# Kernel optimization log

Measured on AMD Instinct MI355X. Metric: run time of the kernel, lower is better.

Reference implementation:

```python
import jax, jax.numpy as jnp
import numpy as np

N = 50000      # num nodes
E = 800000     # num edges
F = 64         # in_channels
H = 4          # heads
C = 64         # out_channels
NEG_SLOPE = 0.2
SCALE = float(np.sqrt(F))  # scaled_product=True -> divide by sqrt(in_channels)


def setup_inputs() -> dict:
    key = jax.random.key(0)
    k1, k2, k3, k4, k5, k6 = jax.random.split(key, 6)
    x = jax.random.normal(k1, (N, F), dtype=jnp.float32)
    edge_index = jax.random.randint(k2, (2, E), 0, N, dtype=jnp.int32)
    edge_weight = jax.random.uniform(k3, (E, 1), dtype=jnp.float32)
    # learned parameters (glorot-ish scale)
    W_lin = jax.random.normal(k4, (F, H * C), dtype=jnp.float32) / np.sqrt(F)
    W_att = jax.random.normal(k5, (F, H * F), dtype=jnp.float32) / np.sqrt(F)
    bias = jnp.zeros((H * C,), dtype=jnp.float32)
    return {"x": x, "edge_index": edge_index, "edge_weight": edge_weight,
            "W_lin": W_lin, "W_att": W_att, "bias": bias}


def reference(x, edge_index, edge_weight, W_lin, W_att, bias):
    src = edge_index[0]  # j: source / message sender
    dst = edge_index[1]  # i: target / aggregation index

    # node transforms
    xs = (x @ W_lin).reshape(N, H, C)   # lin(x): values for messages
    u = (x @ W_att).reshape(N, H, F)    # lin_att(x): multiplicative attention keys

    # multiplicative attention score: x_j^T W_h x_i  -> [E, H]
    score = jnp.einsum('ehf,ef->eh', u[src], x[dst]) / SCALE
    score = jax.nn.leaky_relu(score, NEG_SLOPE)

    # masked scatter-softmax over incoming edges of each destination node
    smax = jax.ops.segment_max(jax.lax.stop_gradient(score), dst, num_segments=N)  # [N, H]
    e = jnp.exp(score - smax[dst]) * edge_weight                                   # mask = edge_weight
    denom = jax.ops.segment_sum(e, dst, num_segments=N) + 1e-16                    # [N, H]
    alpha = e / denom[dst]                                                         # [E, H]

    # message = alpha * x_src, aggregate (add) at destination
    out = jax.ops.segment_sum(alpha[:, :, None] * xs[src], dst, num_segments=N)    # [N, H, C]
    out = out.reshape(N, H * C) + bias                                             # concat heads + bias
    return out
```

## Files before the change

kernel.cpp:

```cpp
#include <hip/hip_runtime.h>
#include <hip/hip_bf16.h>
#include <math.h>

#define N_NODES 50000
#define N_EDGES 800000
#define GEMM_ROWS 32
#define AGG_NODES 32
#define CSR_STRIDE 64
#define SCAT_BLOCKS ((N_EDGES + 1023) / 1024)
#define QGEMM_BLOCKS ((N_NODES + GEMM_ROWS - 1) / GEMM_ROWS)
#define SCALE_FOLD 0.18033688011112042f
#define XT_STRIDE 34

typedef __attribute__((ext_vector_type(8))) short bf16x8_t;
typedef __attribute__((ext_vector_type(4))) float f32x4_t;

static __device__ __forceinline__ ushort bfrn(float v) {
  __hip_bfloat16 b = __float2bfloat16(v);
  return __builtin_bit_cast(ushort, b);
}
static __device__ __forceinline__ bf16x8_t as_bf16x8(uint4 u) {
  union { uint4 a; bf16x8_t b; } c; c.a = u; return c.b;
}
static __device__ __forceinline__ float bflo(uint u) {
  return __uint_as_float(u << 16);
}
static __device__ __forceinline__ float bfhi(uint u) {
  return __uint_as_float(u & 0xFFFF0000u);
}

__global__ __launch_bounds__(256) void init_kernel(
    int* __restrict__ deg, const float* __restrict__ Watt,
    float* __restrict__ Wt) {
  int i = blockIdx.x * 256 + threadIdx.x;
  if (i < N_NODES) deg[i] = 0;
  if (i < 16384) {
    int c = i & 63;
    int r = (i >> 6) & 63;
    int h = i >> 12;
    Wt[i] = Watt[c * 256 + h * 64 + r] * SCALE_FOLD;
  }
}

__global__ __launch_bounds__(256) void combo_kernel(
    const int* __restrict__ srcv, const int* __restrict__ dstv,
    const float* __restrict__ ew, int* __restrict__ deg,
    int2* __restrict__ csr2, const float* __restrict__ x,
    const float* __restrict__ Wt, uint2* __restrict__ q_t2,
    ushort* __restrict__ xhi) {
  const int tid = threadIdx.x;
  if (blockIdx.x < SCAT_BLOCKS) {
    const int e0 = blockIdx.x * 1024 + tid * 4;
    if (e0 + 3 < N_EDGES) {
      const int4 d4 = *(const int4*)(dstv + e0);
      const int4 s4 = *(const int4*)(srcv + e0);
      const float4 w4 = *(const float4*)(ew + e0);
      int p0 = atomicAdd(&deg[d4.x], 1);
      int p1 = atomicAdd(&deg[d4.y], 1);
      int p2 = atomicAdd(&deg[d4.z], 1);
      int p3 = atomicAdd(&deg[d4.w], 1);
      p0 = min(p0, CSR_STRIDE - 1);
      p1 = min(p1, CSR_STRIDE - 1);
      p2 = min(p2, CSR_STRIDE - 1);
      p3 = min(p3, CSR_STRIDE - 1);
      csr2[(size_t)d4.x * CSR_STRIDE + p0] =
          make_int2(s4.x, __float_as_int(w4.x));
      csr2[(size_t)d4.y * CSR_STRIDE + p1] =
          make_int2(s4.y, __float_as_int(w4.y));
      csr2[(size_t)d4.z * CSR_STRIDE + p2] =
          make_int2(s4.z, __float_as_int(w4.z));
      csr2[(size_t)d4.w * CSR_STRIDE + p3] =
          make_int2(s4.w, __float_as_int(w4.w));
    }
    return;
  }
  __shared__ float xlds[GEMM_ROWS * 64];
  const int blk = blockIdx.x - SCAT_BLOCKS;
#pragma unroll
  for (int p = 0; p < 8; ++p) {
    int idx = p * 256 + tid;
    int gidx = blk * (GEMM_ROWS * 64) + idx;
    xlds[idx] = (gidx < N_NODES * 64) ? x[gidx] : 0.f;
  }
  __syncthreads();
  {
    int row = tid >> 3;
    int c0 = (tid & 7) * 8;
    int grow = blk * GEMM_ROWS + row;
    if (grow < N_NODES) {
      uint hu[4];
#pragma unroll
      for (int d2 = 0; d2 < 4; ++d2) {
        float v0 = xlds[row * 64 + c0 + 2 * d2];
        float v1 = xlds[row * 64 + c0 + 2 * d2 + 1];
        hu[d2] = (uint)bfrn(v0) | ((uint)bfrn(v1) << 16);
      }
      *(uint4*)(xhi + (size_t)grow * 64 + c0) =
          make_uint4(hu[0], hu[1], hu[2], hu[3]);
    }
  }
  const int c4 = tid & 63;
  const int h = c4 >> 4;
  const int f4 = c4 & 15;
  const int rg = (tid >> 6) * 8;
  const float4* Wv = (const float4*)Wt;
  float4 acc[8] = {};
  for (int g = 0; g < 64; ++g) {
    float4 w4 = Wv[(size_t)h * 1024 + g * 16 + f4];
#pragma unroll
    for (int r = 0; r < 8; ++r) {
      float a = xlds[(rg + r) * 64 + g];
      acc[r].x += a * w4.x; acc[r].y += a * w4.y;
      acc[r].z += a * w4.z; acc[r].w += a * w4.w;
    }
  }
#pragma unroll
  for (int r = 0; r < 8; ++r) {
    int row = blk * GEMM_ROWS + rg + r;
    if (row < N_NODES) {
      uint2 pk;
      pk.x = (uint)bfrn(acc[r].x) | ((uint)bfrn(acc[r].y) << 16);
      pk.y = (uint)bfrn(acc[r].z) | ((uint)bfrn(acc[r].w) << 16);
      q_t2[(size_t)row * 64 + c4] = pk;
    }
  }
}

__global__ __launch_bounds__(256) void aggregate_kernel(
    const uint4* __restrict__ qt4, const uint4* __restrict__ xhi4,
    const int* __restrict__ deg, const int2* __restrict__ csr2,
    ushort* __restrict__ agg) {
  __shared__ __attribute__((aligned(16))) ushort xt16[4][16][XT_STRIDE * 2];
  __shared__ __attribute__((aligned(16))) ushort pt[4][4][16];
  const int wave = threadIdx.x >> 6;
  const int node = blockIdx.x * 4 + wave;
  const int lane = threadIdx.x & 63;
  const int l15 = lane & 15;
  const int lg = lane >> 4;
  const int hq = l15 & 3;

  const bf16x8_t Qa = as_bf16x8(qt4[(size_t)node * 32 + hq * 8 + lg]);
  const bf16x8_t Qb = as_bf16x8(qt4[(size_t)node * 32 + hq * 8 + 4 + lg]);
  int d = deg[node];
  d = min(d, CSR_STRIDE);
  const int ntiles = (d + 15) >> 4;
  const int s0 = node * CSR_STRIDE;

  const bf16x8_t ONES =
      as_bf16x8(make_uint4(0x3F803F80u, 0x3F803F80u, 0x3F803F80u, 0x3F803F80u));
  f32x4_t acc0 = {0.f, 0.f, 0.f, 0.f};
  f32x4_t acc1 = {0.f, 0.f, 0.f, 0.f};
  f32x4_t acc2 = {0.f, 0.f, 0.f, 0.f};
  f32x4_t acc3 = {0.f, 0.f, 0.f, 0.f};
  f32x4_t accL = {0.f, 0.f, 0.f, 0.f};
  const int eb = (lg & 1) * 8;

  for (int t = 0; t < ntiles; ++t) {
    const int k0 = s0 + t * 16;
    const int2 e2 = csr2[k0 + l15];
    const bool valid = (t * 16 + l15) < d;
    const float w = valid ? __int_as_float(e2.y) : 0.f;
    const uint j = min((uint)e2.x, (uint)(N_NODES - 1));
    const uint4 ah0 = xhi4[(size_t)j * 8 + lg];
    const uint4 ah1 = xhi4[(size_t)j * 8 + 4 + lg];
    {
      ushort* xr = &xt16[wave][l15][0];
      *(uint2*)(xr + 8 * lg) = make_uint2(ah0.x, ah0.y);
      *(uint2*)(xr + 8 * lg + 4) = make_uint2(ah0.z, ah0.w);
      *(uint2*)(xr + 32 + 8 * lg) = make_uint2(ah1.x, ah1.y);
      *(uint2*)(xr + 32 + 8 * lg + 4) = make_uint2(ah1.z, ah1.w);
    }
    f32x4_t S = {0.f, 0.f, 0.f, 0.f};
    S = __builtin_amdgcn_mfma_f32_16x16x32_bf16(Qa, as_bf16x8(ah0), S, 0, 0, 0);
    S = __builtin_amdgcn_mfma_f32_16x16x32_bf16(Qb, as_bf16x8(ah1), S, 0, 0, 0);
    float p0 = exp2f(fmaxf(S[0], 0.2f * S[0])) * w;
    float p1 = exp2f(fmaxf(S[1], 0.2f * S[1])) * w;
    float p2 = exp2f(fmaxf(S[2], 0.2f * S[2])) * w;
    float p3 = exp2f(fmaxf(S[3], 0.2f * S[3])) * w;
    if (lg == 0) {
      pt[wave][0][l15] = bfrn(p0);
      pt[wave][1][l15] = bfrn(p1);
      pt[wave][2][l15] = bfrn(p2);
      pt[wave][3][l15] = bfrn(p3);
    }
    uint4 pau = make_uint4(0u, 0u, 0u, 0u);
    if (lg < 2) pau = *(const uint4*)&pt[wave][hq][8 * lg];
    const bf16x8_t pa = as_bf16x8(pau);
#pragma unroll
    for (int b = 0; b < 4; ++b) {
      const int fc = 16 * b + l15;
      uint bw0 = (uint)xt16[wave][eb + 0][fc] |
                 ((uint)xt16[wave][eb + 1][fc] << 16);
      uint bw1 = (uint)xt16[wave][eb + 2][fc] |
                 ((uint)xt16[wave][eb + 3][fc] << 16);
      uint bw2 = (uint)xt16[wave][eb + 4][fc] |
                 ((uint)xt16[wave][eb + 5][fc] << 16);
      uint bw3 = (uint)xt16[wave][eb + 6][fc] |
                 ((uint)xt16[wave][eb + 7][fc] << 16);
      const bf16x8_t bx = as_bf16x8(make_uint4(bw0, bw1, bw2, bw3));
      if (b == 0)
        acc0 = __builtin_amdgcn_mfma_f32_16x16x32_bf16(pa, bx, acc0, 0, 0, 0);
      else if (b == 1)
        acc1 = __builtin_amdgcn_mfma_f32_16x16x32_bf16(pa, bx, acc1, 0, 0, 0);
      else if (b == 2)
        acc2 = __builtin_amdgcn_mfma_f32_16x16x32_bf16(pa, bx, acc2, 0, 0, 0);
      else
        acc3 = __builtin_amdgcn_mfma_f32_16x16x32_bf16(pa, bx, acc3, 0, 0, 0);
    }
    accL = __builtin_amdgcn_mfma_f32_16x16x32_bf16(pa, ONES, accL, 0, 0, 0);
  }

  const float lpv = (lg == 0) ? accL[0]
                  : (lg == 1) ? accL[1]
                  : (lg == 2) ? accL[2] : accL[3];
  const float inv = 1.f / (lpv + 1e-16f);
  const float v0 = ((lg == 0) ? acc0[0] : (lg == 1) ? acc0[1]
                   : (lg == 2) ? acc0[2] : acc0[3]) * inv;
  const float v1 = ((lg == 0) ? acc1[0] : (lg == 1) ? acc1[1]
                   : (lg == 2) ? acc1[2] : acc1[3]) * inv;
  const float v2 = ((lg == 0) ? acc2[0] : (lg == 1) ? acc2[1]
                   : (lg == 2) ? acc2[2] : acc2[3]) * inv;
  const float v3 = ((lg == 0) ? acc3[0] : (lg == 1) ? acc3[1]
                   : (lg == 2) ? acc3[2] : acc3[3]) * inv;
  ushort* ap = agg + (size_t)node * 256 + lg * 64 + l15;
  ap[0] = bfrn(v0);
  ap[16] = bfrn(v1);
  ap[32] = bfrn(v2);
  ap[48] = bfrn(v3);
}

__global__ __launch_bounds__(256) void out_gemm_kernel(
    const ushort* __restrict__ agg, const float* __restrict__ Wlin,
    const float* __restrict__ bias, float* __restrict__ out) {
  __shared__ float4 atile[AGG_NODES][4][17];
  const int tid = threadIdx.x;
  const int node0 = blockIdx.x * AGG_NODES;
  const uint2* av = (const uint2*)agg;
#pragma unroll
  for (int p = 0; p < 8; ++p) {
    int idx = p * 256 + tid;
    int row = idx >> 6;
    int cc = idx & 63;
    if (node0 + row < N_NODES) {
      uint2 u = av[(size_t)(node0 + row) * 64 + cc];
      float4 f;
      f.x = bflo(u.x); f.y = bfhi(u.x);
      f.z = bflo(u.y); f.w = bfhi(u.y);
      atile[row][cc >> 4][cc & 15] = f;
    }
  }
  __syncthreads();
  const int c4 = tid & 63;
  const int ns = tid >> 6;
  const int hh = c4 >> 4;
  const float4* Wv = (const float4*)Wlin;
  float4 acc[8] = {};
  for (int g4 = 0; g4 < 16; ++g4) {
    float4 w0 = Wv[(size_t)(g4 * 4 + 0) * 64 + c4];
    float4 w1 = Wv[(size_t)(g4 * 4 + 1) * 64 + c4];
    float4 w2 = Wv[(size_t)(g4 * 4 + 2) * 64 + c4];
    float4 w3 = Wv[(size_t)(g4 * 4 + 3) * 64 + c4];
#pragma unroll
    for (int n = 0; n < 8; ++n) {
      float4 a = atile[ns * 8 + n][hh][g4];
      acc[n].x += a.x * w0.x + a.y * w1.x + a.z * w2.x + a.w * w3.x;
      acc[n].y += a.x * w0.y + a.y * w1.y + a.z * w2.y + a.w * w3.y;
      acc[n].z += a.x * w0.z + a.y * w1.z + a.z * w2.z + a.w * w3.z;
      acc[n].w += a.x * w0.w + a.y * w1.w + a.z * w2.w + a.w * w3.w;
    }
  }
  float4 bv = ((const float4*)bias)[c4];
#pragma unroll
  for (int n = 0; n < 8; ++n) {
    int node = node0 + ns * 8 + n;
    if (node < N_NODES) {
      float4 o;
      o.x = acc[n].x + bv.x; o.y = acc[n].y + bv.y;
      o.z = acc[n].z + bv.z; o.w = acc[n].w + bv.w;
      ((float4*)out)[(size_t)node * 64 + c4] = o;
    }
  }
}

extern "C" void kernel_launch(void* const* d_in, const int* in_sizes, int n_in,
                              void* d_out, int out_size, void* d_ws,
                              size_t ws_size, hipStream_t stream) {
  (void)in_sizes; (void)n_in; (void)out_size; (void)ws_size;
  const float* x    = (const float*)d_in[0];
  const int*   ei   = (const int*)d_in[1];
  const float* ew   = (const float*)d_in[2];
  const float* Wlin = (const float*)d_in[3];
  const float* Watt = (const float*)d_in[4];
  const float* bias = (const float*)d_in[5];
  float* out = (float*)d_out;

  const int* srcv = ei;
  const int* dstv = ei + N_EDGES;

  char* ws = (char*)d_ws;
  size_t off = 0;
  auto alloc = [&](size_t bytes) {
    void* p = ws + off;
    off += (bytes + 255) & ~(size_t)255;
    return p;
  };
  ushort* q_t  = (ushort*)alloc((size_t)N_NODES * 256 * 2);
  ushort* agg  = (ushort*)alloc((size_t)N_NODES * 256 * 2);
  ushort* xhi  = (ushort*)alloc((size_t)N_NODES * 64 * 2);
  int2*   csr2 = (int2*)alloc((size_t)N_NODES * CSR_STRIDE * 8);
  int*    deg  = (int*)alloc((size_t)N_NODES * 4);
  float*  Wt   = (float*)alloc((size_t)64 * 256 * 4);

  init_kernel<<<(N_NODES + 255) / 256, 256, 0, stream>>>(deg, Watt, Wt);
  combo_kernel<<<SCAT_BLOCKS + QGEMM_BLOCKS, 256, 0, stream>>>(
      srcv, dstv, ew, deg, csr2, x, Wt, (uint2*)q_t, xhi);
  aggregate_kernel<<<N_NODES / 4, 256, 0, stream>>>(
      (const uint4*)q_t, (const uint4*)xhi, deg, csr2, agg);
  out_gemm_kernel<<<(N_NODES + AGG_NODES - 1) / AGG_NODES, 256, 0, stream>>>(
      agg, Wlin, bias, out);
}
```

Before: 159.5 us.

## Pack CSR source index and fp16 weight into one word; split scatter and qgemm

Each CSR entry shrinks from an 8-byte (int src, float weight) pair to a 4-byte word: a 16-bit source index plus an fp16 edge weight. This halves the bytes written by the scatter and read by the aggregation. The fused scatter/q-GEMM kernel is split into two separate launches, which gives up their overlap inside one grid. The q-GEMM inner loop now reads four x values per float4 LDS access. The 16-bit index only works because N_NODES is below 65536, and fp16 weights lose some precision.

```diff
diff --git a/kernel.cpp b/kernel.cpp
--- a/kernel.cpp
+++ b/kernel.cpp
@@ -27,6 +27,13 @@
 }
 static __device__ __forceinline__ float bfhi(uint u) {
   return __uint_as_float(u & 0xFFFF0000u);
+}
+static __device__ __forceinline__ uint pack_sw(int s, float w) {
+  ushort hw = __builtin_bit_cast(ushort, (_Float16)w);
+  return (uint)s | ((uint)hw << 16);
+}
+static __device__ __forceinline__ float unpack_w(uint pk) {
+  return (float)__builtin_bit_cast(_Float16, (ushort)(pk >> 16));
 }
 
 __global__ __launch_bounds__(256) void init_kernel(
@@ -42,40 +49,35 @@
   }
 }
 
-__global__ __launch_bounds__(256) void combo_kernel(
+__global__ __launch_bounds__(256) void scatter_kernel(
     const int* __restrict__ srcv, const int* __restrict__ dstv,
     const float* __restrict__ ew, int* __restrict__ deg,
-    int2* __restrict__ csr2, const float* __restrict__ x,
-    const float* __restrict__ Wt, uint2* __restrict__ q_t2,
-    ushort* __restrict__ xhi) {
+    uint* __restrict__ csr_p) {
+  const int e0 = blockIdx.x * 1024 + threadIdx.x * 4;
+  if (e0 + 3 >= N_EDGES) return;
+  const int4 d4 = *(const int4*)(dstv + e0);
+  const int4 s4 = *(const int4*)(srcv + e0);
+  const float4 w4 = *(const float4*)(ew + e0);
+  int p0 = atomicAdd(&deg[d4.x], 1);
+  int p1 = atomicAdd(&deg[d4.y], 1);
+  int p2 = atomicAdd(&deg[d4.z], 1);
+  int p3 = atomicAdd(&deg[d4.w], 1);
+  p0 = min(p0, CSR_STRIDE - 1);
+  p1 = min(p1, CSR_STRIDE - 1);
+  p2 = min(p2, CSR_STRIDE - 1);
+  p3 = min(p3, CSR_STRIDE - 1);
+  csr_p[(size_t)d4.x * CSR_STRIDE + p0] = pack_sw(s4.x, w4.x);
+  csr_p[(size_t)d4.y * CSR_STRIDE + p1] = pack_sw(s4.y, w4.y);
+  csr_p[(size_t)d4.z * CSR_STRIDE + p2] = pack_sw(s4.z, w4.z);
+  csr_p[(size_t)d4.w * CSR_STRIDE + p3] = pack_sw(s4.w, w4.w);
+}
+
+__global__ __launch_bounds__(256) void qgemm_kernel(
+    const float* __restrict__ x, const float* __restrict__ Wt,
+    uint2* __restrict__ q_t2, ushort* __restrict__ xhi) {
+  __shared__ float xlds[GEMM_ROWS * 64];
   const int tid = threadIdx.x;
-  if (blockIdx.x < SCAT_BLOCKS) {
-    const int e0 = blockIdx.x * 1024 + tid * 4;
-    if (e0 + 3 < N_EDGES) {
-      const int4 d4 = *(const int4*)(dstv + e0);
-      const int4 s4 = *(const int4*)(srcv + e0);
-      const float4 w4 = *(const float4*)(ew + e0);
-      int p0 = atomicAdd(&deg[d4.x], 1);
-      int p1 = atomicAdd(&deg[d4.y], 1);
-      int p2 = atomicAdd(&deg[d4.z], 1);
-      int p3 = atomicAdd(&deg[d4.w], 1);
-      p0 = min(p0, CSR_STRIDE - 1);
-      p1 = min(p1, CSR_STRIDE - 1);
-      p2 = min(p2, CSR_STRIDE - 1);
-      p3 = min(p3, CSR_STRIDE - 1);
-      csr2[(size_t)d4.x * CSR_STRIDE + p0] =
-          make_int2(s4.x, __float_as_int(w4.x));
-      csr2[(size_t)d4.y * CSR_STRIDE + p1] =
-          make_int2(s4.y, __float_as_int(w4.y));
-      csr2[(size_t)d4.z * CSR_STRIDE + p2] =
-          make_int2(s4.z, __float_as_int(w4.z));
-      csr2[(size_t)d4.w * CSR_STRIDE + p3] =
-          make_int2(s4.w, __float_as_int(w4.w));
-    }
-    return;
-  }
-  __shared__ float xlds[GEMM_ROWS * 64];
-  const int blk = blockIdx.x - SCAT_BLOCKS;
+  const int blk = blockIdx.x;
 #pragma unroll
   for (int p = 0; p < 8; ++p) {
     int idx = p * 256 + tid;
@@ -104,14 +106,20 @@
   const int f4 = c4 & 15;
   const int rg = (tid >> 6) * 8;
   const float4* Wv = (const float4*)Wt;
+  const float4* xv4 = (const float4*)xlds;
   float4 acc[8] = {};
-  for (int g = 0; g < 64; ++g) {
-    float4 w4 = Wv[(size_t)h * 1024 + g * 16 + f4];
+  for (int g4 = 0; g4 < 16; ++g4) {
+    float4 w0 = Wv[(size_t)h * 1024 + (g4 * 4 + 0) * 16 + f4];
+    float4 w1 = Wv[(size_t)h * 1024 + (g4 * 4 + 1) * 16 + f4];
+    float4 w2 = Wv[(size_t)h * 1024 + (g4 * 4 + 2) * 16 + f4];
+    float4 w3 = Wv[(size_t)h * 1024 + (g4 * 4 + 3) * 16 + f4];
 #pragma unroll
     for (int r = 0; r < 8; ++r) {
-      float a = xlds[(rg + r) * 64 + g];
-      acc[r].x += a * w4.x; acc[r].y += a * w4.y;
-      acc[r].z += a * w4.z; acc[r].w += a * w4.w;
+      float4 xa = xv4[(rg + r) * 16 + g4];
+      acc[r].x += xa.x * w0.x + xa.y * w1.x + xa.z * w2.x + xa.w * w3.x;
+      acc[r].y += xa.x * w0.y + xa.y * w1.y + xa.z * w2.y + xa.w * w3.y;
+      acc[r].z += xa.x * w0.z + xa.y * w1.z + xa.z * w2.z + xa.w * w3.z;
+      acc[r].w += xa.x * w0.w + xa.y * w1.w + xa.z * w2.w + xa.w * w3.w;
     }
   }
 #pragma unroll
@@ -128,7 +136,7 @@
 
 __global__ __launch_bounds__(256) void aggregate_kernel(
     const uint4* __restrict__ qt4, const uint4* __restrict__ xhi4,
-    const int* __restrict__ deg, const int2* __restrict__ csr2,
+    const int* __restrict__ deg, const uint* __restrict__ csr_p,
     ushort* __restrict__ agg) {
   __shared__ __attribute__((aligned(16))) ushort xt16[4][16][XT_STRIDE * 2];
   __shared__ __attribute__((aligned(16))) ushort pt[4][4][16];
@@ -157,10 +165,10 @@
 
   for (int t = 0; t < ntiles; ++t) {
     const int k0 = s0 + t * 16;
-    const int2 e2 = csr2[k0 + l15];
+    const uint pk = csr_p[k0 + l15];
     const bool valid = (t * 16 + l15) < d;
-    const float w = valid ? __int_as_float(e2.y) : 0.f;
-    const uint j = min((uint)e2.x, (uint)(N_NODES - 1));
+    const float w = valid ? unpack_w(pk) : 0.f;
+    const uint j = min(pk & 0xFFFFu, (uint)(N_NODES - 1));
     const uint4 ah0 = xhi4[(size_t)j * 8 + lg];
     const uint4 ah1 = xhi4[(size_t)j * 8 + 4 + lg];
     {
@@ -304,18 +312,18 @@
     off += (bytes + 255) & ~(size_t)255;
     return p;
   };
-  ushort* q_t  = (ushort*)alloc((size_t)N_NODES * 256 * 2);
-  ushort* agg  = (ushort*)alloc((size_t)N_NODES * 256 * 2);
-  ushort* xhi  = (ushort*)alloc((size_t)N_NODES * 64 * 2);
-  int2*   csr2 = (int2*)alloc((size_t)N_NODES * CSR_STRIDE * 8);
-  int*    deg  = (int*)alloc((size_t)N_NODES * 4);
-  float*  Wt   = (float*)alloc((size_t)64 * 256 * 4);
+  ushort* q_t   = (ushort*)alloc((size_t)N_NODES * 256 * 2);
+  ushort* agg   = (ushort*)alloc((size_t)N_NODES * 256 * 2);
+  ushort* xhi   = (ushort*)alloc((size_t)N_NODES * 64 * 2);
+  uint*   csr_p = (uint*)alloc((size_t)N_NODES * CSR_STRIDE * 4);
+  int*    deg   = (int*)alloc((size_t)N_NODES * 4);
+  float*  Wt    = (float*)alloc((size_t)64 * 256 * 4);
 
   init_kernel<<<(N_NODES + 255) / 256, 256, 0, stream>>>(deg, Watt, Wt);
-  combo_kernel<<<SCAT_BLOCKS + QGEMM_BLOCKS, 256, 0, stream>>>(
-      srcv, dstv, ew, deg, csr2, x, Wt, (uint2*)q_t, xhi);
+  scatter_kernel<<<SCAT_BLOCKS, 256, 0, stream>>>(srcv, dstv, ew, deg, csr_p);
+  qgemm_kernel<<<QGEMM_BLOCKS, 256, 0, stream>>>(x, Wt, (uint2*)q_t, xhi);
   aggregate_kernel<<<N_NODES / 4, 256, 0, stream>>>(
-      (const uint4*)q_t, (const uint4*)xhi, deg, csr2, agg);
+      (const uint4*)q_t, (const uint4*)xhi, deg, csr_p, agg);
   out_gemm_kernel<<<(N_NODES + AGG_NODES - 1) / AGG_NODES, 256, 0, stream>>>(
       agg, Wlin, bias, out);
 }
```

Measured after the change: 156.2 us, median of 2. 2.1% less time.
